# Kernel tuning notes

Hardware: AMD Instinct MI355X
Metric: run time of the kernel (lower is better)

The kernel has to match this reference:

```python
import jax, jax.numpy as jnp
import numpy as np


def _maxpool(x, win):
    return jax.lax.reduce_window(x, -jnp.inf, jax.lax.max, (1, 1) + win, (1, 1, 1, 1, 1), 'SAME')


def dilation26(x):
    return _maxpool(x, (3, 3, 3))


def dilation6(x):
    p1 = _maxpool(x, (3, 1, 1))
    p2 = _maxpool(x, (1, 3, 1))
    p3 = _maxpool(x, (1, 1, 3))
    return jnp.maximum(jnp.maximum(p1, p2), p3)


def erosion6(x):
    return -dilation6(-x)


def skeletonize3d(X, iters):
    # opening3d(X, conn_e=6, conn_d=26) = dilation26(erosion6(X)); persistent=True
    skel = jax.nn.relu(X - dilation26(erosion6(X)))
    for _ in range(iters):
        Xe = erosion6(X)
        delta = jax.nn.relu(Xe - dilation26(erosion6(Xe)))
        skel = X * dilation26(skel) + skel          # persistent reinforcement
        skel = skel + delta - skel * delta
        X = Xe
    # skel[skel>1] = skel/skel.detach() -> numerically 1.0
    return jnp.where(skel > 1.0, jnp.asarray(1.0, skel.dtype), skel)


def persistent_skeletonization3d(X, niter):
    return skeletonize3d(skeletonize3d(X, niter), niter // 2)


def _bmean_vs(v, s, eps):
    ax = (1, 2, 3, 4)
    return jnp.mean((jnp.sum(v * s, axis=ax) + eps) / (jnp.sum(s, axis=ax) + eps))


def ms_loss(Vlogit, Vcl, Vedt, k=5, eps=1e-12, bin_tresh=0.7):
    Vp = jax.nn.sigmoid(Vlogit)
    Vb = (jax.lax.stop_gradient(Vp) > bin_tresh).astype(Vp.dtype)
    Vb = jnp.pad(Vb, ((0, 0), (0, 0), (3, 3), (3, 3), (3, 3)), constant_values=1.0)
    S = persistent_skeletonization3d(Vb, k)[:, :, 3:-3, 3:-3, 3:-3]
    Sp = jax.lax.stop_gradient(S) * Vp
    tprec = _bmean_vs(Vp, Vcl, eps)
    tsens = _bmean_vs(Vcl, Sp, eps)
    return 1.0 - (2.0 * tprec * tsens + eps) / (tprec + tsens + eps)


def setup_inputs() -> dict:
    key = jax.random.key(0)
    k1, k2, k3 = jax.random.split(key, 3)
    B, C, D, H, W = 2, 1, 128, 128, 128
    Vlogit = jax.random.normal(k1, (B, C, D, H, W), dtype=jnp.float32)
    Vcl = jax.random.uniform(k2, (B, C, D, H, W), dtype=jnp.float32)
    Vedt = jax.random.uniform(k3, (B, C, D, H, W), dtype=jnp.float32)
    return {"Vlogit": Vlogit, "Vcl": Vcl, "Vedt": Vedt}


def reference(Vlogit, Vcl, Vedt):
    return ms_loss(Vlogit, Vcl, Vedt, k=5, eps=1e-12, bin_tresh=0.7)
```

## Files before the change

### kernel.cpp

```cpp
#include <hip/hip_runtime.h>
#include <stdint.h>

typedef unsigned long long u64;

#define PADW 134
#define WPR 3
#define ROWS_PER_B (PADW * PADW)
#define WPB (ROWS_PER_B * WPR)
#define NBATCH 2
#define NROWS (NBATCH * ROWS_PER_B)
#define NWORDS (NBATCH * WPB)
#define NV 128
#define NV3 (NV * NV * NV)
#define PAD 3


__device__ __forceinline__ bool inR(int v) { return (unsigned)v < (unsigned)PADW; }

__device__ __forceinline__ void loadRow(const u64* __restrict__ B, int z, int y, u64 r[3]) {
  const u64* p = B + (z * PADW + y) * WPR;
  r[0] = p[0]; r[1] = p[1]; r[2] = p[2];
}

__device__ __forceinline__ void orHdil(const u64 r[3], u64 d[3]) {
  d[0] |= r[0] | (r[0] << 1) | ((r[0] >> 1) | (r[1] << 63));
  d[1] |= r[1] | ((r[1] << 1) | (r[0] >> 63)) | ((r[1] >> 1) | (r[2] << 63));
  d[2] |= r[2] | ((r[2] << 1) | (r[1] >> 63)) | (r[2] >> 1);
}

__device__ __forceinline__ void eroX(const u64 c[3], u64 e[3]) {
  e[0] = c[0] & ((c[0] << 1) | 1ULL)        & ((c[0] >> 1) | (c[1] << 63));
  e[1] = c[1] & ((c[1] << 1) | (c[0] >> 63)) & ((c[1] >> 1) | (c[2] << 63));
  e[2] = c[2] & ((c[2] << 1) | (c[1] >> 63)) & ((c[2] >> 1) | (1ULL << 5));
}

__device__ __forceinline__ void ridDecomp(int rid, int& b, int& z, int& y) {
  b = rid / ROWS_PER_B;
  int r = rid - b * ROWS_PER_B;
  z = r / PADW;
  y = r - z * PADW;
}

__global__ void binpack_k(const float* __restrict__ logit, u64* __restrict__ X) {
  int wid = (blockIdx.x * blockDim.x + threadIdx.x) >> 6;
  int lane = threadIdx.x & 63;
  if (wid >= NROWS) return;
  int b, z, y;
  ridDecomp(wid, b, z, y);
  bool padrow = (z < PAD || z >= PAD + NV || y < PAD || y >= PAD + NV);
  const float TH = 0.84729786f;
  u64* rowp = X + (size_t)b * WPB + (z * PADW + y) * WPR;
#pragma unroll
  for (int j = 0; j < WPR; ++j) {
    int x = j * 64 + lane;
    bool pred = false;
    if (x < PADW) {
      if (padrow || x < PAD || x >= PAD + NV) {
        pred = true;
      } else {
        float l = logit[(((size_t)b * NV + (z - PAD)) * NV + (y - PAD)) * NV + (x - PAD)];
        pred = l > TH;
      }
    }
    u64 w = __ballot(pred);
    if (lane == 0) rowp[j] = w;
  }
}

__global__ void ero_k(const u64* __restrict__ in, u64* __restrict__ out) {
  int rid = blockIdx.x * blockDim.x + threadIdx.x;
  if (rid >= NROWS) return;
  int b, z, y;
  ridDecomp(rid, b, z, y);
  const u64* Bb = in + (size_t)b * WPB;
  u64 c[3], e[3], n[3];
  loadRow(Bb, z, y, c);
  eroX(c, e);
  if (inR(y - 1)) { loadRow(Bb, z, y - 1, n); e[0] &= n[0]; e[1] &= n[1]; e[2] &= n[2]; }
  if (inR(y + 1)) { loadRow(Bb, z, y + 1, n); e[0] &= n[0]; e[1] &= n[1]; e[2] &= n[2]; }
  if (inR(z - 1)) { loadRow(Bb, z - 1, y, n); e[0] &= n[0]; e[1] &= n[1]; e[2] &= n[2]; }
  if (inR(z + 1)) { loadRow(Bb, z + 1, y, n); e[0] &= n[0]; e[1] &= n[1]; e[2] &= n[2]; }
  u64* o = out + (size_t)b * WPB + (z * PADW + y) * WPR;
  o[0] = e[0]; o[1] = e[1]; o[2] = e[2];
}

__global__ void open_init2_k(const u64* __restrict__ X, const u64* __restrict__ E1,
                             u64* __restrict__ sk, u64* __restrict__ E2) {
  int rid = blockIdx.x * blockDim.x + threadIdx.x;
  if (rid >= NROWS) return;
  int b, z, y;
  ridDecomp(rid, b, z, y);
  size_t boff = (size_t)b * WPB;
  const u64* Eb = E1 + boff;
  u64 acc[3] = {0, 0, 0};
  u64 cc[3];
  u64 cy0[3] = {~0ULL, ~0ULL, ~0ULL}, cy1[3] = {~0ULL, ~0ULL, ~0ULL};
  u64 cz0[3] = {~0ULL, ~0ULL, ~0ULL}, cz1[3] = {~0ULL, ~0ULL, ~0ULL};
#pragma unroll
  for (int dz = -1; dz <= 1; ++dz) {
#pragma unroll
    for (int dy = -1; dy <= 1; ++dy) {
      int zz = z + dz, yy = y + dy;
      if (!inR(zz) || !inR(yy)) continue;
      u64 t[3];
      loadRow(Eb, zz, yy, t);
      orHdil(t, acc);
      if (dz == 0 && dy == 0) { cc[0] = t[0]; cc[1] = t[1]; cc[2] = t[2]; }
      else if (dz == 0 && dy == -1) { cy0[0] = t[0]; cy0[1] = t[1]; cy0[2] = t[2]; }
      else if (dz == 0 && dy == 1)  { cy1[0] = t[0]; cy1[1] = t[1]; cy1[2] = t[2]; }
      else if (dz == -1 && dy == 0) { cz0[0] = t[0]; cz0[1] = t[1]; cz0[2] = t[2]; }
      else if (dz == 1 && dy == 0)  { cz1[0] = t[0]; cz1[1] = t[1]; cz1[2] = t[2]; }
    }
  }
  u64 xr[3];
  loadRow(X + boff, z, y, xr);
  u64 e[3];
  eroX(cc, e);
#pragma unroll
  for (int j = 0; j < 3; ++j) e[j] &= cy0[j] & cy1[j] & cz0[j] & cz1[j];
  int rw = (z * PADW + y) * WPR;
#pragma unroll
  for (int j = 0; j < 3; ++j) {
    sk[boff + rw + j] = xr[j] & ~acc[j];
    E2[boff + rw + j] = e[j];
  }
}

__global__ void update2_k(const u64* __restrict__ X, const u64* __restrict__ E1,
                          const u64* __restrict__ E2, const u64* __restrict__ sk,
                          u64* __restrict__ sk2, u64* __restrict__ E3) {
  int rid = blockIdx.x * blockDim.x + threadIdx.x;
  if (rid >= NROWS) return;
  int b, z, y;
  ridDecomp(rid, b, z, y);
  size_t boff = (size_t)b * WPB;
  const u64* Eb = E2 + boff;
  const u64* Sb = sk + boff;
  u64 acc[3] = {0, 0, 0}, dsk[3] = {0, 0, 0};
  u64 cc[3], skc[3];
  u64 cy0[3] = {~0ULL, ~0ULL, ~0ULL}, cy1[3] = {~0ULL, ~0ULL, ~0ULL};
  u64 cz0[3] = {~0ULL, ~0ULL, ~0ULL}, cz1[3] = {~0ULL, ~0ULL, ~0ULL};
#pragma unroll
  for (int dz = -1; dz <= 1; ++dz) {
#pragma unroll
    for (int dy = -1; dy <= 1; ++dy) {
      int zz = z + dz, yy = y + dy;
      if (!inR(zz) || !inR(yy)) continue;
      u64 t[3], s[3];
      loadRow(Eb, zz, yy, t);
      loadRow(Sb, zz, yy, s);
      orHdil(t, acc);
      orHdil(s, dsk);
      if (dz == 0 && dy == 0) {
        cc[0] = t[0]; cc[1] = t[1]; cc[2] = t[2];
        skc[0] = s[0]; skc[1] = s[1]; skc[2] = s[2];
      }
      else if (dz == 0 && dy == -1) { cy0[0] = t[0]; cy0[1] = t[1]; cy0[2] = t[2]; }
      else if (dz == 0 && dy == 1)  { cy1[0] = t[0]; cy1[1] = t[1]; cy1[2] = t[2]; }
      else if (dz == -1 && dy == 0) { cz0[0] = t[0]; cz0[1] = t[1]; cz0[2] = t[2]; }
      else if (dz == 1 && dy == 0)  { cz1[0] = t[0]; cz1[1] = t[1]; cz1[2] = t[2]; }
    }
  }
  u64 e1r[3], xr[3];
  loadRow(E1 + boff, z, y, e1r);
  loadRow(X + boff, z, y, xr);
  u64 e[3];
  eroX(cc, e);
#pragma unroll
  for (int j = 0; j < 3; ++j) e[j] &= cy0[j] & cy1[j] & cz0[j] & cz1[j];
  int rw = (z * PADW + y) * WPR;
#pragma unroll
  for (int j = 0; j < 3; ++j) {
    u64 delta = e1r[j] & ~acc[j];
    u64 s1 = (xr[j] & dsk[j]) | skc[j];
    sk2[boff + rw + j] = delta | s1;
    E3[boff + rw + j] = e[j];
  }
}

__global__ void reduce_k(const float* __restrict__ logit, const float* __restrict__ vcl,
                         const u64* __restrict__ S, double* __restrict__ acc) {
  int b = blockIdx.y;
  const float* lg = logit + (size_t)b * NV3;
  const float* cl = vcl + (size_t)b * NV3;
  const u64* Sb = S + (size_t)b * WPB;
  float p0 = 0.f, p1 = 0.f, p2 = 0.f, p3 = 0.f;
  for (int i = blockIdx.x * blockDim.x + threadIdx.x; i < NV3; i += gridDim.x * blockDim.x) {
    int z = i >> 14;
    int r = i & 16383;
    int y = r >> 7;
    int x = r & 127;
    float vp = 1.0f / (1.0f + expf(-lg[i]));
    float c = cl[i];
    p0 += vp * c;
    p1 += c;
    int xp = x + PAD;
    u64 w = Sb[((z + PAD) * PADW + (y + PAD)) * WPR + (xp >> 6)];
    if ((w >> (xp & 63)) & 1ULL) {
      p2 += c * vp;
      p3 += vp;
    }
  }
  for (int off = 32; off > 0; off >>= 1) {
    p0 += __shfl_down(p0, off);
    p1 += __shfl_down(p1, off);
    p2 += __shfl_down(p2, off);
    p3 += __shfl_down(p3, off);
  }
  __shared__ float s0[4], s1[4], s2[4], s3[4];
  int wid = threadIdx.x >> 6;
  int lane = threadIdx.x & 63;
  if (lane == 0) { s0[wid] = p0; s1[wid] = p1; s2[wid] = p2; s3[wid] = p3; }
  __syncthreads();
  if (threadIdx.x == 0) {
    double a0 = 0, a1 = 0, a2 = 0, a3 = 0;
    for (int w = 0; w < 4; ++w) { a0 += s0[w]; a1 += s1[w]; a2 += s2[w]; a3 += s3[w]; }
    atomicAdd(&acc[b * 4 + 0], a0);
    atomicAdd(&acc[b * 4 + 1], a1);
    atomicAdd(&acc[b * 4 + 2], a2);
    atomicAdd(&acc[b * 4 + 3], a3);
  }
}

__global__ void finalize_k(const double* __restrict__ acc, float* __restrict__ out) {
  if (threadIdx.x != 0 || blockIdx.x != 0) return;
  const double eps = 1e-12;
  double tp = 0.5 * ((acc[0] + eps) / (acc[1] + eps) + (acc[4] + eps) / (acc[5] + eps));
  double ts = 0.5 * ((acc[2] + eps) / (acc[3] + eps) + (acc[6] + eps) / (acc[7] + eps));
  double loss = 1.0 - (2.0 * tp * ts + eps) / (tp + ts + eps);
  out[0] = (float)loss;
}

extern "C" void kernel_launch(void* const* d_in, const int* in_sizes, int n_in,
                              void* d_out, int out_size, void* d_ws, size_t ws_size,
                              hipStream_t stream) {
  const float* logit = (const float*)d_in[0];
  const float* vcl = (const float*)d_in[1];
  float* out = (float*)d_out;

  const size_t bufW = (size_t)NWORDS;
  u64* base = (u64*)d_ws;
  u64* B[7];
  for (int i = 0; i < 7; ++i) B[i] = base + (size_t)i * bufW;
  double* acc = (double*)(base + 7 * bufW);

  const int mThreads = 64;
  const int mBlocks = (NROWS + mThreads - 1) / mThreads;
  const int bBlocks = (NROWS + 3) / 4;

  binpack_k<<<bBlocks, 256, 0, stream>>>(logit, B[0]);

  u64 *X = B[0], *E1 = B[1], *E2 = B[2], *E3 = B[3], *sk = B[4], *sk2 = B[5];
  ero_k<<<mBlocks, mThreads, 0, stream>>>(X, E1);
  open_init2_k<<<mBlocks, mThreads, 0, stream>>>(X, E1, sk, E2);
  for (int it = 0; it < 5; ++it) {
    update2_k<<<mBlocks, mThreads, 0, stream>>>(X, E1, E2, sk, sk2, E3);
    u64* t = X; X = E1; E1 = E2; E2 = E3; E3 = t;
    t = sk; sk = sk2; sk2 = t;
  }
  u64* S1 = sk;

  u64 *X2 = S1, *E1b = B[6], *E2b = X, *E3b = E1, *skb = E2, *sk2b = E3;
  ero_k<<<mBlocks, mThreads, 0, stream>>>(X2, E1b);
  open_init2_k<<<mBlocks, mThreads, 0, stream>>>(X2, E1b, skb, E2b);
  for (int it = 0; it < 2; ++it) {
    update2_k<<<mBlocks, mThreads, 0, stream>>>(X2, E1b, E2b, skb, sk2b, E3b);
    u64* t = X2; X2 = E1b; E1b = E2b; E2b = E3b; E3b = t;
    t = skb; skb = sk2b; sk2b = t;
  }
  u64* Sfinal = skb;

  hipMemsetAsync(acc, 0, 8 * sizeof(double), stream);
  reduce_k<<<dim3(256, 2), 256, 0, stream>>>(logit, vcl, Sfinal, acc);
  finalize_k<<<1, 64, 0, stream>>>(acc, out);
}
```

Baseline: 187.1 us.

## Fuse memset and finalize into neighboring kernels and vectorize reduction

The accumulator zeroing moves into binpack_k, and the finalize step moves into reduce_k through a last-block counter, which removes a memset and a kernel launch. reduce_k now runs one float4 per thread across both batches with 2048 blocks, replacing the grid-stride scalar loop, and turns the skeleton-bit branch into a multiply. The price is more global atomics (8 per block over many more blocks) and a threadfence/counter protocol that must be correct for the final read.

```diff
diff --git a/kernel.cpp b/kernel.cpp
--- a/kernel.cpp
+++ b/kernel.cpp
@@ -41,7 +41,13 @@
   y = r - z * PADW;
 }
 
-__global__ void binpack_k(const float* __restrict__ logit, u64* __restrict__ X) {
+__global__ void binpack_k(const float* __restrict__ logit, u64* __restrict__ X,
+                          double* __restrict__ acc, unsigned* __restrict__ cnt) {
+  if (blockIdx.x == 0 && threadIdx.x == 0) {
+#pragma unroll
+    for (int k = 0; k < 8; ++k) acc[k] = 0.0;
+    *cnt = 0u;
+  }
   int wid = (blockIdx.x * blockDim.x + threadIdx.x) >> 6;
   int lane = threadIdx.x & 63;
   if (wid >= NROWS) return;
@@ -178,57 +184,67 @@
   }
 }
 
-__global__ void reduce_k(const float* __restrict__ logit, const float* __restrict__ vcl,
-                         const u64* __restrict__ S, double* __restrict__ acc) {
-  int b = blockIdx.y;
-  const float* lg = logit + (size_t)b * NV3;
-  const float* cl = vcl + (size_t)b * NV3;
-  const u64* Sb = S + (size_t)b * WPB;
-  float p0 = 0.f, p1 = 0.f, p2 = 0.f, p3 = 0.f;
-  for (int i = blockIdx.x * blockDim.x + threadIdx.x; i < NV3; i += gridDim.x * blockDim.x) {
-    int z = i >> 14;
-    int r = i & 16383;
-    int y = r >> 7;
-    int x = r & 127;
-    float vp = 1.0f / (1.0f + expf(-lg[i]));
-    float c = cl[i];
-    p0 += vp * c;
-    p1 += c;
-    int xp = x + PAD;
-    u64 w = Sb[((z + PAD) * PADW + (y + PAD)) * WPR + (xp >> 6)];
-    if ((w >> (xp & 63)) & 1ULL) {
-      p2 += c * vp;
-      p3 += vp;
-    }
-  }
-  for (int off = 32; off > 0; off >>= 1) {
-    p0 += __shfl_down(p0, off);
-    p1 += __shfl_down(p1, off);
-    p2 += __shfl_down(p2, off);
-    p3 += __shfl_down(p3, off);
-  }
-  __shared__ float s0[4], s1[4], s2[4], s3[4];
-  int wid = threadIdx.x >> 6;
-  int lane = threadIdx.x & 63;
-  if (lane == 0) { s0[wid] = p0; s1[wid] = p1; s2[wid] = p2; s3[wid] = p3; }
+__global__ __launch_bounds__(256, 8) void reduce_k(const float* __restrict__ logit,
+                                                   const float* __restrict__ vcl,
+                                                   const u64* __restrict__ S,
+                                                   double* __restrict__ acc,
+                                                   unsigned* __restrict__ cnt,
+                                                   float* __restrict__ out) {
+  int t = blockIdx.x * 256 + threadIdx.x;
+  int i = t << 2;
+  int z = i >> 14, y = (i >> 7) & 127, x = i & 127;
+  float p[8];
+#pragma unroll
+  for (int k = 0; k < 8; ++k) p[k] = 0.f;
+#pragma unroll
+  for (int b = 0; b < NBATCH; ++b) {
+    float4 lv = ((const float4*)(logit + (size_t)b * NV3))[t];
+    float4 cv = ((const float4*)(vcl + (size_t)b * NV3))[t];
+    const u64* rowp = S + (size_t)b * WPB + ((size_t)(z + PAD) * PADW + (y + PAD)) * WPR;
+    float lf[4] = {lv.x, lv.y, lv.z, lv.w};
+    float cf[4] = {cv.x, cv.y, cv.z, cv.w};
+#pragma unroll
+    for (int k = 0; k < 4; ++k) {
+      float vp = 1.0f / (1.0f + expf(-lf[k]));
+      int xp = x + k + PAD;
+      u64 w = rowp[xp >> 6];
+      float s = (float)((w >> (xp & 63)) & 1ULL);
+      float c = cf[k];
+      p[b * 4 + 0] += vp * c;
+      p[b * 4 + 1] += c;
+      p[b * 4 + 2] += c * vp * s;
+      p[b * 4 + 3] += vp * s;
+    }
+  }
+#pragma unroll
+  for (int k = 0; k < 8; ++k)
+    for (int off = 32; off > 0; off >>= 1) p[k] += __shfl_down(p[k], off);
+  __shared__ float ls[4][8];
+  int wid = threadIdx.x >> 6, lane = threadIdx.x & 63;
+  if (lane == 0) {
+#pragma unroll
+    for (int k = 0; k < 8; ++k) ls[wid][k] = p[k];
+  }
   __syncthreads();
   if (threadIdx.x == 0) {
-    double a0 = 0, a1 = 0, a2 = 0, a3 = 0;
-    for (int w = 0; w < 4; ++w) { a0 += s0[w]; a1 += s1[w]; a2 += s2[w]; a3 += s3[w]; }
-    atomicAdd(&acc[b * 4 + 0], a0);
-    atomicAdd(&acc[b * 4 + 1], a1);
-    atomicAdd(&acc[b * 4 + 2], a2);
-    atomicAdd(&acc[b * 4 + 3], a3);
-  }
-}
-
-__global__ void finalize_k(const double* __restrict__ acc, float* __restrict__ out) {
-  if (threadIdx.x != 0 || blockIdx.x != 0) return;
-  const double eps = 1e-12;
-  double tp = 0.5 * ((acc[0] + eps) / (acc[1] + eps) + (acc[4] + eps) / (acc[5] + eps));
-  double ts = 0.5 * ((acc[2] + eps) / (acc[3] + eps) + (acc[6] + eps) / (acc[7] + eps));
-  double loss = 1.0 - (2.0 * tp * ts + eps) / (tp + ts + eps);
-  out[0] = (float)loss;
+#pragma unroll
+    for (int k = 0; k < 8; ++k) {
+      double a = (double)ls[0][k] + ls[1][k] + ls[2][k] + ls[3][k];
+      atomicAdd(&acc[k], a);
+    }
+    __threadfence();
+    unsigned old = atomicAdd(cnt, 1u);
+    if (old == gridDim.x - 1) {
+      __threadfence();
+      double a[8];
+#pragma unroll
+      for (int k = 0; k < 8; ++k) a[k] = atomicAdd(&acc[k], 0.0);
+      const double eps = 1e-12;
+      double tp = 0.5 * ((a[0] + eps) / (a[1] + eps) + (a[4] + eps) / (a[5] + eps));
+      double ts = 0.5 * ((a[2] + eps) / (a[3] + eps) + (a[6] + eps) / (a[7] + eps));
+      out[0] = (float)(1.0 - (2.0 * tp * ts + eps) / (tp + ts + eps));
+    }
+  }
 }
 
 extern "C" void kernel_launch(void* const* d_in, const int* in_sizes, int n_in,
@@ -243,12 +259,13 @@
   u64* B[7];
   for (int i = 0; i < 7; ++i) B[i] = base + (size_t)i * bufW;
   double* acc = (double*)(base + 7 * bufW);
+  unsigned* cnt = (unsigned*)(acc + 8);
 
   const int mThreads = 64;
   const int mBlocks = (NROWS + mThreads - 1) / mThreads;
   const int bBlocks = (NROWS + 3) / 4;
 
-  binpack_k<<<bBlocks, 256, 0, stream>>>(logit, B[0]);
+  binpack_k<<<bBlocks, 256, 0, stream>>>(logit, B[0], acc, cnt);
 
   u64 *X = B[0], *E1 = B[1], *E2 = B[2], *E3 = B[3], *sk = B[4], *sk2 = B[5];
   ero_k<<<mBlocks, mThreads, 0, stream>>>(X, E1);
@@ -270,7 +287,5 @@
   }
   u64* Sfinal = skb;
 
-  hipMemsetAsync(acc, 0, 8 * sizeof(double), stream);
-  reduce_k<<<dim3(256, 2), 256, 0, stream>>>(logit, vcl, Sfinal, acc);
-  finalize_k<<<1, 64, 0, stream>>>(acc, out);
-}
+  reduce_k<<<524288 / 256, 256, 0, stream>>>(logit, vcl, Sfinal, acc, cnt, out);
+}
```

Measured after the change: 356.0 us. 90.3% more time.
